# Performance work log

Measured on AMD Instinct MI355X. Metric: run time of the kernel, lower is better.

## Reference

```python
import jax, jax.numpy as jnp
import numpy as np

THRESHOLD = 1e-3  # hardcoded `thresholds = 0.001` in the sparse branch


def setup_inputs() -> dict:
    key = jax.random.key(0)
    k1, k2, k3, k4, k5 = jax.random.split(key, 5)
    b, r, d_in, d_out = 8, 4096, 768, 768
    x = jax.random.normal(k1, (b, r, d_in), dtype=jnp.float32)
    weight = jax.random.normal(k2, (d_out, d_in), dtype=jnp.float32) * 0.02
    bias = jax.random.normal(k3, (d_out,), dtype=jnp.float32) * 0.02
    U = jax.random.normal(k4, (d_in, d_in), dtype=jnp.float32) * (d_in ** -0.5)
    VT = jax.random.normal(k5, (d_out, d_out), dtype=jnp.float32) * (d_out ** -0.5)
    return {"x": x, "weight": weight, "bias": bias, "U": U, "VT": VT}


def reference(x, weight, bias, U, VT):
    # Sparse path (len_grads >= 30) of LinearFunctionSparseGrad.forward.
    # h = x @ U.T, rotated into the gradient basis.  [b, r, c]
    h = jnp.einsum('brc,dc->brd', x, U)
    # Threshold-sparsify: zero entries with |h| <= 0.001.
    h = jnp.where(jnp.abs(h) > THRESHOLD, h, jnp.zeros((), h.dtype))
    # Original: gather nonzero rows/cols, h[rows][:, cols] @ weight.T[cols],
    # then scatter back via I[:, rows] @ res_. Dropped cols are exactly-zero
    # columns and dropped rows are exactly-zero rows, so the math equals a
    # dense matmul on the masked tensor (no [b*r, b*r] identity needed).
    res = jnp.einsum('brc,oc->bro', h, weight)        # h @ weight.T
    res = jnp.einsum('bro,po->brp', res, VT)          # res_ @ VT.T (self.VT=VT_orig.T => VT here)
    return res + bias
```

## Files before the change

### kernel.cpp

```cpp
#include <hip/hip_runtime.h>
#include <hip/hip_bf16.h>

typedef __bf16 bf16_t;
typedef bf16_t bf16x8 __attribute__((ext_vector_type(8)));
typedef bf16_t bf16x4 __attribute__((ext_vector_type(4)));
typedef float  f32x4  __attribute__((ext_vector_type(4)));

#define BM 256
#define BN 128
#define BK 64

enum { EPI_NONE = 0, EPI_THRESH = 1, EPI_BIAS = 2 };

__device__ __forceinline__ void memfence() { asm volatile("" ::: "memory"); }
__device__ __forceinline__ void blockbar() {
    memfence(); __builtin_amdgcn_s_barrier(); memfence();
}

#define GLD16(src, dst) __builtin_amdgcn_global_load_lds( \
    (const __attribute__((address_space(1))) void*)(src), \
    (__attribute__((address_space(3))) void*)(dst), 16, 0, 0)

template <int EPI, typename CT>
__device__ __forceinline__
void gemm_tile(const bf16_t* __restrict__ A, const bf16_t* __restrict__ B,
               CT* __restrict__ C, const float* __restrict__ bias,
               int m0, int n0, int N, int K,
               bf16_t* __restrict__ As, bf16_t* __restrict__ Bs)
{
    const int lane = threadIdx.x & 63;
    const int wave = threadIdx.x >> 6;
    const int wm = wave >> 1;
    const int wn = wave & 1;

    const int fm  = lane & 15;
    const int q   = lane >> 4;
    const int fsw = fm & 7;

    const int NT = K / BK;

    const bf16_t* gsrc[6];
    int ldst[6];
#pragma unroll
    for (int s = 0; s < 6; ++s) {
        const int g = wave + 8 * s;
        if (s < 4) {
            const int u = g * 64 + lane;
            const int row = u >> 3;
            const int ch  = (u & 7) ^ (row & 7);
            gsrc[s] = A + (size_t)(m0 + row) * K + ch * 8;
            ldst[s] = g * 512;
        } else {
            const int u = (g - 32) * 64 + lane;
            const int row = u >> 3;
            const int ch  = (u & 7) ^ (row & 7);
            gsrc[s] = B + (size_t)(n0 + row) * K + ch * 8;
            ldst[s] = (g - 32) * 512;
        }
    }

    f32x4 acc[4][4];
#pragma unroll
    for (int i = 0; i < 4; ++i)
#pragma unroll
        for (int j = 0; j < 4; ++j) acc[i][j] = (f32x4){0.f, 0.f, 0.f, 0.f};

#pragma unroll
    for (int s = 0; s < 6; ++s) {
        GLD16(gsrc[s], (s < 4 ? As : Bs) + ldst[s]);
        gsrc[s] += BK;
    }
#pragma unroll
    for (int s = 0; s < 6; ++s) {
        GLD16(gsrc[s], (s < 4 ? As + 256 * 64 : Bs + 128 * 64) + ldst[s]);
        gsrc[s] += BK;
    }
    asm volatile("s_waitcnt vmcnt(6)" ::: "memory");
    blockbar();

    int bc = 0;
    for (int t = 0; t < NT; ++t) {
        const bf16_t* __restrict__ Ab = As + bc * (256 * 64);
        const bf16_t* __restrict__ Bb = Bs + bc * (128 * 64);
        const int bs2 = (bc >= 1) ? bc - 1 : 2;
        bf16_t* Asd = As + bs2 * (256 * 64);
        bf16_t* Bsd = Bs + bs2 * (128 * 64);
        const bool do_stage = (t + 2 < NT);

        bf16x8 af[4][2], bfr[2][2];

#pragma unroll
        for (int i = 0; i < 4; ++i) {
            const int row = wm * 64 + i * 16 + fm;
#pragma unroll
            for (int kk = 0; kk < 2; ++kk)
                af[i][kk] = *(const bf16x8*)(Ab + (size_t)(row * 8 + ((kk * 4 + q) ^ fsw)) * 8);
        }
#pragma unroll
        for (int j = 0; j < 2; ++j) {
            const int row = wn * 64 + j * 16 + fm;
#pragma unroll
            for (int kk = 0; kk < 2; ++kk)
                bfr[j][kk] = *(const bf16x8*)(Bb + (size_t)(row * 8 + ((kk * 4 + q) ^ fsw)) * 8);
        }
        if (do_stage) {
            GLD16(gsrc[0], Asd + ldst[0]); gsrc[0] += BK;
            GLD16(gsrc[1], Asd + ldst[1]); gsrc[1] += BK;
            GLD16(gsrc[4], Bsd + ldst[4]); gsrc[4] += BK;
        }
        blockbar();
        __builtin_amdgcn_s_setprio(1);
#pragma unroll
        for (int i = 0; i < 4; ++i)
#pragma unroll
            for (int j = 0; j < 2; ++j)
#pragma unroll
                for (int kk = 0; kk < 2; ++kk)
                    acc[i][j] = __builtin_amdgcn_mfma_f32_16x16x32_bf16(
                        af[i][kk], bfr[j][kk], acc[i][j], 0, 0, 0);
        __builtin_amdgcn_s_setprio(0);
        blockbar();

#pragma unroll
        for (int j = 0; j < 2; ++j) {
            const int row = wn * 64 + (j + 2) * 16 + fm;
#pragma unroll
            for (int kk = 0; kk < 2; ++kk)
                bfr[j][kk] = *(const bf16x8*)(Bb + (size_t)(row * 8 + ((kk * 4 + q) ^ fsw)) * 8);
        }
        if (do_stage) {
            GLD16(gsrc[2], Asd + ldst[2]); gsrc[2] += BK;
            GLD16(gsrc[3], Asd + ldst[3]); gsrc[3] += BK;
            GLD16(gsrc[5], Bsd + ldst[5]); gsrc[5] += BK;
        }
        blockbar();
        __builtin_amdgcn_s_setprio(1);
#pragma unroll
        for (int i = 0; i < 4; ++i)
#pragma unroll
            for (int j = 0; j < 2; ++j)
#pragma unroll
                for (int kk = 0; kk < 2; ++kk)
                    acc[i][j + 2] = __builtin_amdgcn_mfma_f32_16x16x32_bf16(
                        af[i][kk], bfr[j][kk], acc[i][j + 2], 0, 0, 0);
        __builtin_amdgcn_s_setprio(0);

        if (t < NT - 1) {
            asm volatile("s_waitcnt lgkmcnt(0)" ::: "memory");
            if (do_stage) asm volatile("s_waitcnt vmcnt(6)" ::: "memory");
            else          asm volatile("s_waitcnt vmcnt(0)" ::: "memory");
            blockbar();
        }
        bc = (bc >= 2) ? 0 : bc + 1;
    }

#pragma unroll
    for (int i = 0; i < 4; ++i) {
#pragma unroll
        for (int j = 0; j < 4; ++j) {
            const int col = n0 + wn * 64 + j * 16 + fm;
            float bv = 0.f;
            if (EPI == EPI_BIAS) bv = bias[col];
#pragma unroll
            for (int r = 0; r < 4; ++r) {
                const int row = m0 + wm * 64 + i * 16 + q * 4 + r;
                float v = acc[i][j][r];
                if (EPI == EPI_THRESH) v = (fabsf(v) > 1e-3f) ? v : 0.f;
                if (EPI == EPI_BIAS) v += bv;
                C[(size_t)row * N + col] = (CT)v;
            }
        }
    }
}

__global__ __launch_bounds__(512, 2)
void gemm_h_wc(const bf16_t* __restrict__ xb, const bf16_t* __restrict__ Ub,
               bf16_t* __restrict__ h,
               const bf16_t* __restrict__ VTb, const bf16_t* __restrict__ Wt,
               bf16_t* __restrict__ Wc)
{
    __shared__ __align__(16) bf16_t As[3 * 256 * 64];
    __shared__ __align__(16) bf16_t Bs[3 * 128 * 64];
    const int b = blockIdx.x;
    if (b < 768) {
        const int L = (b & 7) * 96 + (b >> 3);
        gemm_tile<EPI_THRESH, bf16_t>(xb, Ub, h, nullptr,
                                      (L / 6) * BM, (L % 6) * BN, 768, 768, As, Bs);
    } else {
        const int b2 = b - 768;
        gemm_tile<EPI_NONE, bf16_t>(VTb, Wt, Wc, nullptr,
                                    (b2 / 6) * BM, (b2 % 6) * BN, 768, 768, As, Bs);
    }
}

__global__ __launch_bounds__(512, 2)
void gemm_out(const bf16_t* __restrict__ h, const bf16_t* __restrict__ Wc,
              float* __restrict__ out, const float* __restrict__ bias)
{
    __shared__ __align__(16) bf16_t As[3 * 256 * 64];
    __shared__ __align__(16) bf16_t Bs[3 * 128 * 64];
    const int b = blockIdx.x;
    const int L = (b & 7) * 96 + (b >> 3);
    gemm_tile<EPI_BIAS, float>(h, Wc, out, bias,
                               (L / 6) * BM, (L % 6) * BN, 768, 768, As, Bs);
}

__global__ __launch_bounds__(256)
void prep(const float* __restrict__ x, const float* __restrict__ U,
          const float* __restrict__ VT, const float* __restrict__ w,
          bf16_t* __restrict__ xb, bf16_t* __restrict__ Ub,
          bf16_t* __restrict__ VTb, bf16_t* __restrict__ Wt)
{
    __shared__ float tt[32][33];
    const int b = blockIdx.x;
    if (b < 12864) {
        const float* src; bf16_t* dst; size_t e;
        if (b < 12288)      { src = x;  dst = xb;  e = (size_t)b * 2048; }
        else if (b < 12576) { src = U;  dst = Ub;  e = (size_t)(b - 12288) * 2048; }
        else                { src = VT; dst = VTb; e = (size_t)(b - 12576) * 2048; }
        const size_t i = e + (size_t)threadIdx.x * 8;
        const f32x4 v0 = *(const f32x4*)(src + i);
        const f32x4 v1 = *(const f32x4*)(src + i + 4);
        bf16x8 o;
        o[0] = (bf16_t)v0[0]; o[1] = (bf16_t)v0[1];
        o[2] = (bf16_t)v0[2]; o[3] = (bf16_t)v0[3];
        o[4] = (bf16_t)v1[0]; o[5] = (bf16_t)v1[1];
        o[6] = (bf16_t)v1[2]; o[7] = (bf16_t)v1[3];
        *(bf16x8*)(dst + i) = o;
    } else {
        const int t = b - 12864;
        const int bx = (t % 24) * 32, by = (t / 24) * 32;
        const int tx = threadIdx.x & 31, ty = threadIdx.x >> 5;
#pragma unroll
        for (int i = 0; i < 32; i += 8)
            tt[ty + i][tx] = w[(size_t)(by + ty + i) * 768 + bx + tx];
        __syncthreads();
#pragma unroll
        for (int i = 0; i < 32; i += 8)
            Wt[(size_t)(bx + ty + i) * 768 + by + tx] = (bf16_t)tt[tx][ty + i];
    }
}

extern "C" void kernel_launch(void* const* d_in, const int* in_sizes, int n_in,
                              void* d_out, int out_size, void* d_ws, size_t ws_size,
                              hipStream_t stream)
{
    const float* x    = (const float*)d_in[0];
    const float* w    = (const float*)d_in[1];
    const float* bias = (const float*)d_in[2];
    const float* U    = (const float*)d_in[3];
    const float* VT   = (const float*)d_in[4];
    float* out = (float*)d_out;

    const int D = 768;
    const int M = 8 * 4096;
    const size_t MD = (size_t)M * D;
    const size_t DD = (size_t)D * D;

    char* ws = (char*)d_ws;
    bf16_t* xb  = (bf16_t*)ws;
    bf16_t* h   = (bf16_t*)(ws + MD * 2);
    bf16_t* Ub  = (bf16_t*)(ws + MD * 4);
    bf16_t* VTb = (bf16_t*)(ws + MD * 4 + DD * 2);
    bf16_t* Wt  = (bf16_t*)(ws + MD * 4 + DD * 4);
    bf16_t* Wc  = (bf16_t*)(ws + MD * 4 + DD * 6);

    prep<<<13440, 256, 0, stream>>>(x, U, VT, w, xb, Ub, VTb, Wt);
    gemm_h_wc<<<768 + 18, 512, 0, stream>>>(xb, Ub, h, VTb, Wt, Wc);
    gemm_out<<<768, 512, 0, stream>>>(h, Wc, out, bias);
}
```

Measured before the change: 295.4 us.

## Halve GEMM K-tile to 32 and raise occupancy to four blocks per CU

The K-tile shrinks from 64 to 32, so the triple-buffered LDS footprint halves (about 72KB per block) and launch bounds now ask for 4 blocks of 512 threads per CU. The LDS swizzle is reworked for 4 chunks per row, and the per-iteration loop drops from two split MFMA phases with extra barriers to a single phase of 16 MFMAs. The small Wc GEMM blocks are moved to the front of the grid so they are scheduled early. The trade-off is twice as many K iterations, each with a barrier and waitcnt, and tighter register limits at the higher occupancy.

```diff
diff --git a/kernel.cpp b/kernel.cpp
--- a/kernel.cpp
+++ b/kernel.cpp
@@ -8,7 +8,9 @@
 
 #define BM 256
 #define BN 128
-#define BK 64
+#define BK 32
+#define ABUF (BM * BK)
+#define BBUF (BN * BK)
 
 enum { EPI_NONE = 0, EPI_THRESH = 1, EPI_BIAS = 2 };
 
@@ -33,31 +35,33 @@
     const int wm = wave >> 1;
     const int wn = wave & 1;
 
-    const int fm  = lane & 15;
-    const int q   = lane >> 4;
-    const int fsw = fm & 7;
+    const int fm   = lane & 15;
+    const int q    = lane >> 4;
+    const int fsw2 = (fm ^ (fm >> 2)) & 3;
 
     const int NT = K / BK;
 
-    const bf16_t* gsrc[6];
-    int ldst[6];
-#pragma unroll
-    for (int s = 0; s < 6; ++s) {
-        const int g = wave + 8 * s;
-        if (s < 4) {
-            const int u = g * 64 + lane;
-            const int row = u >> 3;
-            const int ch  = (u & 7) ^ (row & 7);
-            gsrc[s] = A + (size_t)(m0 + row) * K + ch * 8;
-            ldst[s] = g * 512;
-        } else {
-            const int u = (g - 32) * 64 + lane;
-            const int row = u >> 3;
-            const int ch  = (u & 7) ^ (row & 7);
-            gsrc[s] = B + (size_t)(n0 + row) * K + ch * 8;
-            ldst[s] = (g - 32) * 512;
-        }
-    }
+    const bf16_t* ga0; const bf16_t* ga1; const bf16_t* gb;
+    {
+        const int u0 = (wave * 2) * 64 + lane;
+        const int r0 = u0 >> 2;
+        ga0 = A + (size_t)(m0 + r0) * K + (((u0 & 3) ^ ((r0 ^ (r0 >> 2)) & 3)) * 8);
+        const int u1 = (wave * 2 + 1) * 64 + lane;
+        const int r1 = u1 >> 2;
+        ga1 = A + (size_t)(m0 + r1) * K + (((u1 & 3) ^ ((r1 ^ (r1 >> 2)) & 3)) * 8);
+        const int ub = wave * 64 + lane;
+        const int rb = ub >> 2;
+        gb  = B + (size_t)(n0 + rb) * K + (((ub & 3) ^ ((rb ^ (rb >> 2)) & 3)) * 8);
+    }
+    const int la0 = wave * 1024;
+    const int la1 = wave * 1024 + 512;
+    const int lb  = wave * 512;
+
+#define STAGE(tt, Ad, Bd) do {                                   \
+    GLD16(ga0 + (size_t)(tt) * BK, (Ad) + la0);                  \
+    GLD16(ga1 + (size_t)(tt) * BK, (Ad) + la1);                  \
+    GLD16(gb  + (size_t)(tt) * BK, (Bd) + lb);                   \
+} while (0)
 
     f32x4 acc[4][4];
 #pragma unroll
@@ -65,89 +69,43 @@
 #pragma unroll
         for (int j = 0; j < 4; ++j) acc[i][j] = (f32x4){0.f, 0.f, 0.f, 0.f};
 
-#pragma unroll
-    for (int s = 0; s < 6; ++s) {
-        GLD16(gsrc[s], (s < 4 ? As : Bs) + ldst[s]);
-        gsrc[s] += BK;
-    }
-#pragma unroll
-    for (int s = 0; s < 6; ++s) {
-        GLD16(gsrc[s], (s < 4 ? As + 256 * 64 : Bs + 128 * 64) + ldst[s]);
-        gsrc[s] += BK;
-    }
-    asm volatile("s_waitcnt vmcnt(6)" ::: "memory");
+    STAGE(0, As, Bs);
+    STAGE(1, As + ABUF, Bs + BBUF);
+    asm volatile("s_waitcnt vmcnt(3)" ::: "memory");
     blockbar();
 
     int bc = 0;
     for (int t = 0; t < NT; ++t) {
-        const bf16_t* __restrict__ Ab = As + bc * (256 * 64);
-        const bf16_t* __restrict__ Bb = Bs + bc * (128 * 64);
+        const bf16_t* __restrict__ Ab = As + bc * ABUF;
+        const bf16_t* __restrict__ Bb = Bs + bc * BBUF;
         const int bs2 = (bc >= 1) ? bc - 1 : 2;
-        bf16_t* Asd = As + bs2 * (256 * 64);
-        bf16_t* Bsd = Bs + bs2 * (128 * 64);
         const bool do_stage = (t + 2 < NT);
 
-        bf16x8 af[4][2], bfr[2][2];
-
+        bf16x8 af[4], bfr[4];
 #pragma unroll
         for (int i = 0; i < 4; ++i) {
             const int row = wm * 64 + i * 16 + fm;
-#pragma unroll
-            for (int kk = 0; kk < 2; ++kk)
-                af[i][kk] = *(const bf16x8*)(Ab + (size_t)(row * 8 + ((kk * 4 + q) ^ fsw)) * 8);
-        }
-#pragma unroll
-        for (int j = 0; j < 2; ++j) {
+            af[i] = *(const bf16x8*)(Ab + (size_t)(row * 4 + (q ^ fsw2)) * 8);
+        }
+#pragma unroll
+        for (int j = 0; j < 4; ++j) {
             const int row = wn * 64 + j * 16 + fm;
-#pragma unroll
-            for (int kk = 0; kk < 2; ++kk)
-                bfr[j][kk] = *(const bf16x8*)(Bb + (size_t)(row * 8 + ((kk * 4 + q) ^ fsw)) * 8);
-        }
-        if (do_stage) {
-            GLD16(gsrc[0], Asd + ldst[0]); gsrc[0] += BK;
-            GLD16(gsrc[1], Asd + ldst[1]); gsrc[1] += BK;
-            GLD16(gsrc[4], Bsd + ldst[4]); gsrc[4] += BK;
-        }
-        blockbar();
+            bfr[j] = *(const bf16x8*)(Bb + (size_t)(row * 4 + (q ^ fsw2)) * 8);
+        }
+        if (do_stage) STAGE(t + 2, As + bs2 * ABUF, Bs + bs2 * BBUF);
+
         __builtin_amdgcn_s_setprio(1);
 #pragma unroll
         for (int i = 0; i < 4; ++i)
 #pragma unroll
-            for (int j = 0; j < 2; ++j)
-#pragma unroll
-                for (int kk = 0; kk < 2; ++kk)
-                    acc[i][j] = __builtin_amdgcn_mfma_f32_16x16x32_bf16(
-                        af[i][kk], bfr[j][kk], acc[i][j], 0, 0, 0);
-        __builtin_amdgcn_s_setprio(0);
-        blockbar();
-
-#pragma unroll
-        for (int j = 0; j < 2; ++j) {
-            const int row = wn * 64 + (j + 2) * 16 + fm;
-#pragma unroll
-            for (int kk = 0; kk < 2; ++kk)
-                bfr[j][kk] = *(const bf16x8*)(Bb + (size_t)(row * 8 + ((kk * 4 + q) ^ fsw)) * 8);
-        }
-        if (do_stage) {
-            GLD16(gsrc[2], Asd + ldst[2]); gsrc[2] += BK;
-            GLD16(gsrc[3], Asd + ldst[3]); gsrc[3] += BK;
-            GLD16(gsrc[5], Bsd + ldst[5]); gsrc[5] += BK;
-        }
-        blockbar();
-        __builtin_amdgcn_s_setprio(1);
-#pragma unroll
-        for (int i = 0; i < 4; ++i)
-#pragma unroll
-            for (int j = 0; j < 2; ++j)
-#pragma unroll
-                for (int kk = 0; kk < 2; ++kk)
-                    acc[i][j + 2] = __builtin_amdgcn_mfma_f32_16x16x32_bf16(
-                        af[i][kk], bfr[j][kk], acc[i][j + 2], 0, 0, 0);
+            for (int j = 0; j < 4; ++j)
+                acc[i][j] = __builtin_amdgcn_mfma_f32_16x16x32_bf16(
+                    af[i], bfr[j], acc[i][j], 0, 0, 0);
         __builtin_amdgcn_s_setprio(0);
 
         if (t < NT - 1) {
             asm volatile("s_waitcnt lgkmcnt(0)" ::: "memory");
-            if (do_stage) asm volatile("s_waitcnt vmcnt(6)" ::: "memory");
+            if (do_stage) asm volatile("s_waitcnt vmcnt(3)" ::: "memory");
             else          asm volatile("s_waitcnt vmcnt(0)" ::: "memory");
             blockbar();
         }
@@ -171,34 +129,35 @@
             }
         }
     }
-}
-
-__global__ __launch_bounds__(512, 2)
+#undef STAGE
+}
+
+__global__ __launch_bounds__(512, 4)
 void gemm_h_wc(const bf16_t* __restrict__ xb, const bf16_t* __restrict__ Ub,
                bf16_t* __restrict__ h,
                const bf16_t* __restrict__ VTb, const bf16_t* __restrict__ Wt,
                bf16_t* __restrict__ Wc)
 {
-    __shared__ __align__(16) bf16_t As[3 * 256 * 64];
-    __shared__ __align__(16) bf16_t Bs[3 * 128 * 64];
+    __shared__ __align__(16) bf16_t As[3 * ABUF];
+    __shared__ __align__(16) bf16_t Bs[3 * BBUF];
     const int b = blockIdx.x;
-    if (b < 768) {
-        const int L = (b & 7) * 96 + (b >> 3);
+    if (b < 18) {
+        gemm_tile<EPI_NONE, bf16_t>(VTb, Wt, Wc, nullptr,
+                                    (b / 6) * BM, (b % 6) * BN, 768, 768, As, Bs);
+    } else {
+        const int bb = b - 18;
+        const int L = (bb & 7) * 96 + (bb >> 3);
         gemm_tile<EPI_THRESH, bf16_t>(xb, Ub, h, nullptr,
                                       (L / 6) * BM, (L % 6) * BN, 768, 768, As, Bs);
-    } else {
-        const int b2 = b - 768;
-        gemm_tile<EPI_NONE, bf16_t>(VTb, Wt, Wc, nullptr,
-                                    (b2 / 6) * BM, (b2 % 6) * BN, 768, 768, As, Bs);
-    }
-}
-
-__global__ __launch_bounds__(512, 2)
+    }
+}
+
+__global__ __launch_bounds__(512, 4)
 void gemm_out(const bf16_t* __restrict__ h, const bf16_t* __restrict__ Wc,
               float* __restrict__ out, const float* __restrict__ bias)
 {
-    __shared__ __align__(16) bf16_t As[3 * 256 * 64];
-    __shared__ __align__(16) bf16_t Bs[3 * 128 * 64];
+    __shared__ __align__(16) bf16_t As[3 * ABUF];
+    __shared__ __align__(16) bf16_t Bs[3 * BBUF];
     const int b = blockIdx.x;
     const int L = (b & 7) * 96 + (b >> 3);
     gemm_tile<EPI_BIAS, float>(h, Wc, out, bias,
@@ -266,6 +225,6 @@
     bf16_t* Wc  = (bf16_t*)(ws + MD * 4 + DD * 6);
 
     prep<<<13440, 256, 0, stream>>>(x, U, VT, w, xb, Ub, VTb, Wt);
-    gemm_h_wc<<<768 + 18, 512, 0, stream>>>(xb, Ub, h, VTb, Wt, Wc);
+    gemm_h_wc<<<18 + 768, 512, 0, stream>>>(xb, Ub, h, VTb, Wt, Wc);
     gemm_out<<<768, 512, 0, stream>>>(h, Wc, out, bias);
 }
```

Measured after the change: 278.0 us. 5.9% less time.
